# Performance work log

Measured on AMD Instinct MI355X. Metric: run time of the kernel, lower is better.

Reference implementation:

```python
import jax, jax.numpy as jnp
import numpy as np

B, L, D, H, DH = 1, 256, 128, 4, 32  # batch, seq, d_pair, n_head, d_hidden


def setup_inputs() -> dict:
    key = jax.random.key(0)
    ks = jax.random.split(key, 8)
    s = 0.02  # init scale for weights
    return {
        "pair": jax.random.normal(ks[0], (B, L, L, D), jnp.float32),
        "ln_w": jnp.ones((D,), jnp.float32),
        "ln_b": jnp.zeros((D,), jnp.float32),
        "Wq": jax.random.normal(ks[1], (D, H * DH), jnp.float32) * s,
        "Wk": jax.random.normal(ks[2], (D, H * DH), jnp.float32) * s,
        "Wv": jax.random.normal(ks[3], (D, H * DH), jnp.float32) * s,
        "Wb": jax.random.normal(ks[4], (D, H), jnp.float32) * s,
        "Wg": jax.random.normal(ks[5], (D, H * DH), jnp.float32) * s,
        "bg": jnp.ones((H * DH,), jnp.float32),
        "Wo": jax.random.normal(ks[6], (H * DH, D), jnp.float32) * s,
        "bo": jnp.zeros((D,), jnp.float32),
    }


def reference(pair, ln_w, ln_b, Wq, Wk, Wv, Wb, Wg, bg, Wo, bo):
    scale = DH ** -0.5
    # LayerNorm over d_pair
    mu = jnp.mean(pair, axis=-1, keepdims=True)
    var = jnp.mean((pair - mu) ** 2, axis=-1, keepdims=True)
    x = (pair - mu) * jax.lax.rsqrt(var + 1e-5) * ln_w + ln_b
    b, l = x.shape[0], x.shape[1]
    bias = jnp.einsum('bijd,dh->bijh', x, Wb)            # (B, L, L, H)
    gate = jax.nn.sigmoid(x @ Wg + bg)                   # (B, L, L, H*DH)
    q = (x @ Wq).reshape(b, l, l, H, DH) * scale
    k = (x @ Wk).reshape(b, l, l, H, DH)
    v = (x @ Wv).reshape(b, l, l, H, DH)
    # triangle attention over k (third L axis), bias shared across i
    attn = jnp.einsum('bijhd,bikhd->bijkh', q, k) + bias[:, None]
    attn = jax.nn.softmax(attn, axis=3)
    out = jnp.einsum('bijkh,bikhd->bijhd', attn, v).reshape(b, l, l, H * DH)
    out = gate * out
    return out @ Wo + bo
```

## Files before the change

### kernel.cpp

```cpp
#include <hip/hip_runtime.h>
#include <math.h>

#define NPOS 65536

typedef _Float16 f16x8 __attribute__((ext_vector_type(8)));
typedef _Float16 f16x4 __attribute__((ext_vector_type(4)));
typedef float    f32x4 __attribute__((ext_vector_type(4)));

__global__ __launch_bounds__(256) void split_w_kernel(
    const float* __restrict__ Wq, const float* __restrict__ Wk,
    const float* __restrict__ Wv, const float* __restrict__ Wg,
    _Float16* __restrict__ Wt_hi, _Float16* __restrict__ Wt_lo)
{
    int t = blockIdx.x * 256 + threadIdx.x;
    int ng = t >> 7, kk = t & 127;
    int mat = ng >> 7, n = ng & 127;
    const float* W = (mat == 0) ? Wq : (mat == 1) ? Wk : (mat == 2) ? Wv : Wg;
    float x = W[kk * 128 + n];
    _Float16 h = (_Float16)x;
    _Float16 lo = (_Float16)((x - (float)h) * 2048.0f);
    Wt_hi[t] = h;
    Wt_lo[t] = lo;
}

__global__ __launch_bounds__(256, 4) void ln_proj_kernel(
    const float* __restrict__ pair, const float* __restrict__ ln_w, const float* __restrict__ ln_b,
    const float* __restrict__ Wb, const float* __restrict__ bg,
    const _Float16* __restrict__ Wt_hi, const _Float16* __restrict__ Wt_lo,
    float* __restrict__ q, float* __restrict__ k, float* __restrict__ v,
    float* __restrict__ g, float* __restrict__ bias_n)
{
    __shared__ _Float16 xbuf[2][64][136];
    _Float16 (*xh)[136] = xbuf[0];
    _Float16 (*xl)[136] = xbuf[1];

    const int tid = threadIdx.x;
    const int p0  = blockIdx.x * 64;
    const int r   = tid >> 2;
    const int cb  = (tid & 3) * 32;

    float xv[32];
    {
        const float4* pr = (const float4*)(pair + (size_t)(p0 + r) * 128 + cb);
        #pragma unroll
        for (int i = 0; i < 8; ++i) {
            float4 t = pr[i];
            xv[i * 4 + 0] = t.x; xv[i * 4 + 1] = t.y;
            xv[i * 4 + 2] = t.z; xv[i * 4 + 3] = t.w;
        }
    }
    float sum = 0.f, sq = 0.f;
    #pragma unroll
    for (int i = 0; i < 32; ++i) { sum += xv[i]; sq += xv[i] * xv[i]; }
    sum += __shfl_xor(sum, 1); sq += __shfl_xor(sq, 1);
    sum += __shfl_xor(sum, 2); sq += __shfl_xor(sq, 2);
    float mean = sum * (1.f / 128.f);
    float var  = sq * (1.f / 128.f) - mean * mean;
    float rstd = rsqrtf(var + 1e-5f);

    float b0 = 0.f, b1 = 0.f, b2 = 0.f, b3 = 0.f;
    #pragma unroll
    for (int i8 = 0; i8 < 4; ++i8) {
        float4 lw0 = *(const float4*)(ln_w + cb + i8 * 8);
        float4 lw1 = *(const float4*)(ln_w + cb + i8 * 8 + 4);
        float4 lb0 = *(const float4*)(ln_b + cb + i8 * 8);
        float4 lb1 = *(const float4*)(ln_b + cb + i8 * 8 + 4);
        float lw[8] = {lw0.x, lw0.y, lw0.z, lw0.w, lw1.x, lw1.y, lw1.z, lw1.w};
        float lb[8] = {lb0.x, lb0.y, lb0.z, lb0.w, lb1.x, lb1.y, lb1.z, lb1.w};
        f16x8 hv, lv;
        #pragma unroll
        for (int j = 0; j < 8; ++j) {
            int i = i8 * 8 + j;
            float xn = (xv[i] - mean) * rstd * lw[j] + lb[j];
            _Float16 h = (_Float16)xn;
            hv[j] = h;
            lv[j] = (_Float16)((xn - (float)h) * 2048.0f);
            float4 wb = *(const float4*)(Wb + (size_t)(cb + i) * 4);
            b0 = fmaf(xn, wb.x, b0); b1 = fmaf(xn, wb.y, b1);
            b2 = fmaf(xn, wb.z, b2); b3 = fmaf(xn, wb.w, b3);
        }
        *(f16x8*)&xh[r][cb + i8 * 8] = hv;
        *(f16x8*)&xl[r][cb + i8 * 8] = lv;
    }
    b0 += __shfl_xor(b0, 1); b1 += __shfl_xor(b1, 1);
    b2 += __shfl_xor(b2, 1); b3 += __shfl_xor(b3, 1);
    b0 += __shfl_xor(b0, 2); b1 += __shfl_xor(b1, 2);
    b2 += __shfl_xor(b2, 2); b3 += __shfl_xor(b3, 2);
    if ((tid & 3) == 0) {
        int p = p0 + r;
        bias_n[0 * NPOS + p] = b0;
        bias_n[1 * NPOS + p] = b1;
        bias_n[2 * NPOS + p] = b2;
        bias_n[3 * NPOS + p] = b3;
    }
    __syncthreads();

    const int w  = tid >> 6, l = tid & 63;
    const int lm = l & 15, lg = l >> 4;
    const int arow = w * 16 + lm;

    f16x8 ahf[4], alf[4];
    #pragma unroll
    for (int kt = 0; kt < 4; ++kt) {
        ahf[kt] = *(const f16x8*)&xh[arow][kt * 32 + lg * 8];
        alf[kt] = *(const f16x8*)&xl[arow][kt * 32 + lg * 8];
    }

    _Float16 (*Bh)[136] = xbuf[0];
    _Float16 (*Bl)[136] = xbuf[1];
    float* stg = (float*)&xbuf[0][0][0];

    const float scale = 0.17677669529663687f;

    for (int chunk = 0; chunk < 8; ++chunk) {
        const int mat = chunk >> 1;
        const int colhalf = (chunk & 1) * 64;
        float* dst = (mat == 0) ? q : (mat == 1) ? k : (mat == 2) ? v : g;

        __syncthreads();

        {
            const _Float16* srch = Wt_hi + (size_t)(chunk * 64) * 128;
            const _Float16* srcl = Wt_lo + (size_t)(chunk * 64) * 128;
            #pragma unroll
            for (int it = 0; it < 4; ++it) {
                int idx = it * 256 + tid;
                int row = idx >> 4, kc8 = (idx & 15) * 8;
                *(f16x8*)&Bh[row][kc8] = *(const f16x8*)(srch + row * 128 + kc8);
                *(f16x8*)&Bl[row][kc8] = *(const f16x8*)(srcl + row * 128 + kc8);
            }
        }
        __syncthreads();

        f32x4 acch[4], accc[4];
        #pragma unroll
        for (int ct = 0; ct < 4; ++ct) {
            acch[ct] = (f32x4){0.f, 0.f, 0.f, 0.f};
            accc[ct] = (f32x4){0.f, 0.f, 0.f, 0.f};
        }
        #pragma unroll
        for (int kt = 0; kt < 4; ++kt) {
            const int koff = kt * 32 + lg * 8;
            #pragma unroll
            for (int ct = 0; ct < 4; ++ct) {
                f16x8 bh = *(const f16x8*)&Bh[ct * 16 + lm][koff];
                f16x8 bl = *(const f16x8*)&Bl[ct * 16 + lm][koff];
                acch[ct] = __builtin_amdgcn_mfma_f32_16x16x32_f16(ahf[kt], bh, acch[ct], 0, 0, 0);
                accc[ct] = __builtin_amdgcn_mfma_f32_16x16x32_f16(alf[kt], bh, accc[ct], 0, 0, 0);
                accc[ct] = __builtin_amdgcn_mfma_f32_16x16x32_f16(ahf[kt], bl, accc[ct], 0, 0, 0);
            }
        }

        __syncthreads();

        #pragma unroll
        for (int ct = 0; ct < 4; ++ct) {
            const int col = ct * 16 + lm;
            float bgv = (mat == 3) ? bg[colhalf + col] : 0.f;
            #pragma unroll
            for (int rr = 0; rr < 4; ++rr) {
                float val = acch[ct][rr] + accc[ct][rr] * (1.0f / 2048.0f);
                if (mat == 0) val *= scale;
                if (mat == 3) val = 1.f / (1.f + __expf(-(val + bgv)));
                stg[(w * 16 + lg * 4 + rr) * 68 + col] = val;
            }
        }
        __syncthreads();

        #pragma unroll
        for (int it = 0; it < 4; ++it) {
            int idx = it * 256 + tid;
            int row = idx >> 4, c4 = (idx & 15) * 4;
            float4 val = *(const float4*)&stg[row * 68 + c4];
            *(float4*)(dst + (size_t)(p0 + row) * 128 + colhalf + c4) = val;
        }
    }
}

__global__ __launch_bounds__(256, 3) void attn_kernel(
    const float* __restrict__ q, const float* __restrict__ k, const float* __restrict__ v,
    const float* __restrict__ g, const float* __restrict__ bias_n, float* __restrict__ go)
{
    __shared__ _Float16 Khs[32][56];
    __shared__ _Float16 Kls[32][56];
    __shared__ _Float16 Vts[32][56];
    __shared__ _Float16 Pb[4][64][40];

    const int tid  = threadIdx.x;
    const int w    = tid >> 6;
    const int lane = tid & 63;
    const int lg   = lane >> 4, lm = lane & 15;
    const int i = blockIdx.x >> 2, h = blockIdx.x & 3;
    const size_t base = (size_t)i * 256 * 128 + (size_t)h * 32;
    const int j0w = w * 64;

    f16x8 qh[4], ql[4];
    #pragma unroll
    for (int jt = 0; jt < 4; ++jt) {
        const float* qp = q + base + (size_t)(j0w + jt * 16 + lm) * 128 + lg * 8;
        float4 a = *(const float4*)qp;
        float4 b = *(const float4*)(qp + 4);
        float qv[8] = {a.x, a.y, a.z, a.w, b.x, b.y, b.z, b.w};
        #pragma unroll
        for (int e = 0; e < 8; ++e) {
            _Float16 hh = (_Float16)qv[e];
            qh[jt][e] = hh;
            ql[jt][e] = (_Float16)((qv[e] - (float)hh) * 2048.0f);
        }
    }

    float Oacc[2][4][4] = {};
    float mrow[4], lrow[4];
    #pragma unroll
    for (int jt = 0; jt < 4; ++jt) { mrow[jt] = -1e30f; lrow[jt] = 0.f; }

    const int sr  = tid >> 3;
    const int sc0 = (tid & 7) * 4;

    float4 kpre = *(const float4*)(k + base + (size_t)sr * 128 + sc0);
    float4 vpre = *(const float4*)(v + base + (size_t)sr * 128 + sc0);

    for (int kc = 0; kc < 256; kc += 32) {
        __syncthreads();
        {
            float kvv[4] = {kpre.x, kpre.y, kpre.z, kpre.w};
            f16x4 h4, l4;
            #pragma unroll
            for (int e = 0; e < 4; ++e) {
                _Float16 hh = (_Float16)kvv[e];
                h4[e] = hh;
                l4[e] = (_Float16)((kvv[e] - (float)hh) * 2048.0f);
            }
            *(f16x4*)&Khs[sr][sc0] = h4;
            *(f16x4*)&Kls[sr][sc0] = l4;
            Vts[sc0 + 0][sr] = (_Float16)vpre.x;
            Vts[sc0 + 1][sr] = (_Float16)vpre.y;
            Vts[sc0 + 2][sr] = (_Float16)vpre.z;
            Vts[sc0 + 3][sr] = (_Float16)vpre.w;
        }
        __syncthreads();
        if (kc + 32 < 256) {
            kpre = *(const float4*)(k + base + (size_t)(kc + 32 + sr) * 128 + sc0);
            vpre = *(const float4*)(v + base + (size_t)(kc + 32 + sr) * 128 + sc0);
        }

        f16x8 bh[2], bl[2], vf[2];
        #pragma unroll
        for (int kt = 0; kt < 2; ++kt) {
            bh[kt] = *(const f16x8*)&Khs[kt * 16 + lm][lg * 8];
            bl[kt] = *(const f16x8*)&Kls[kt * 16 + lm][lg * 8];
            vf[kt] = *(const f16x8*)&Vts[kt * 16 + lm][lg * 8];
        }

        #pragma unroll
        for (int jt = 0; jt < 4; ++jt) {
            const float* bj = bias_n + (size_t)h * NPOS
                            + (size_t)(j0w + jt * 16 + lm) * 256 + kc + lg * 4;
            float4 b0 = *(const float4*)bj;
            float4 b1 = *(const float4*)(bj + 16);
            f32x4 c0h = {b0.x, b0.y, b0.z, b0.w};
            f32x4 c1h = {b1.x, b1.y, b1.z, b1.w};
            f32x4 c0l = {0.f, 0.f, 0.f, 0.f}, c1l = {0.f, 0.f, 0.f, 0.f};
            c0h = __builtin_amdgcn_mfma_f32_16x16x32_f16(bh[0], qh[jt], c0h, 0, 0, 0);
            c0l = __builtin_amdgcn_mfma_f32_16x16x32_f16(bl[0], qh[jt], c0l, 0, 0, 0);
            c0l = __builtin_amdgcn_mfma_f32_16x16x32_f16(bh[0], ql[jt], c0l, 0, 0, 0);
            c1h = __builtin_amdgcn_mfma_f32_16x16x32_f16(bh[1], qh[jt], c1h, 0, 0, 0);
            c1l = __builtin_amdgcn_mfma_f32_16x16x32_f16(bl[1], qh[jt], c1l, 0, 0, 0);
            c1l = __builtin_amdgcn_mfma_f32_16x16x32_f16(bh[1], ql[jt], c1l, 0, 0, 0);

            float s[8];
            #pragma unroll
            for (int rr = 0; rr < 4; ++rr) {
                s[rr]     = c0h[rr] + c0l[rr] * (1.0f / 2048.0f);
                s[4 + rr] = c1h[rr] + c1l[rr] * (1.0f / 2048.0f);
            }
            float mx = s[0];
            #pragma unroll
            for (int e = 1; e < 8; ++e) mx = fmaxf(mx, s[e]);
            mx = fmaxf(mx, __shfl_xor(mx, 16));
            mx = fmaxf(mx, __shfl_xor(mx, 32));
            float mn = fmaxf(mrow[jt], mx);
            float alpha = __expf(mrow[jt] - mn);
            mrow[jt] = mn;
            float p[8], ps = 0.f;
            #pragma unroll
            for (int e = 0; e < 8; ++e) { p[e] = __expf(s[e] - mn); ps += p[e]; }
            ps += __shfl_xor(ps, 16);
            ps += __shfl_xor(ps, 32);
            lrow[jt] = lrow[jt] * alpha + ps;
            #pragma unroll
            for (int dt = 0; dt < 2; ++dt)
                #pragma unroll
                for (int rr = 0; rr < 4; ++rr) Oacc[dt][jt][rr] *= alpha;
            f16x4 pa, pbv;
            #pragma unroll
            for (int rr = 0; rr < 4; ++rr) { pa[rr] = (_Float16)p[rr]; pbv[rr] = (_Float16)p[4 + rr]; }
            *(f16x4*)&Pb[w][jt * 16 + lm][lg * 4]      = pa;
            *(f16x4*)&Pb[w][jt * 16 + lm][16 + lg * 4] = pbv;
        }

        #pragma unroll
        for (int jt = 0; jt < 4; ++jt) {
            f16x8 pf = *(const f16x8*)&Pb[w][jt * 16 + lm][lg * 8];
            #pragma unroll
            for (int dt = 0; dt < 2; ++dt) {
                f32x4 c = {Oacc[dt][jt][0], Oacc[dt][jt][1], Oacc[dt][jt][2], Oacc[dt][jt][3]};
                c = __builtin_amdgcn_mfma_f32_16x16x32_f16(vf[dt], pf, c, 0, 0, 0);
                Oacc[dt][jt][0] = c[0]; Oacc[dt][jt][1] = c[1];
                Oacc[dt][jt][2] = c[2]; Oacc[dt][jt][3] = c[3];
            }
        }
    }

    #pragma unroll
    for (int jt = 0; jt < 4; ++jt) {
        const int j = j0w + jt * 16 + lm;
        const float inv = 1.0f / lrow[jt];
        #pragma unroll
        for (int dt = 0; dt < 2; ++dt) {
            const float* gp = g + base + (size_t)j * 128 + dt * 16 + lg * 4;
            float4 gv = *(const float4*)gp;
            float4 ov;
            ov.x = Oacc[dt][jt][0] * inv * gv.x;
            ov.y = Oacc[dt][jt][1] * inv * gv.y;
            ov.z = Oacc[dt][jt][2] * inv * gv.z;
            ov.w = Oacc[dt][jt][3] * inv * gv.w;
            *(float4*)(go + base + (size_t)j * 128 + dt * 16 + lg * 4) = ov;
        }
    }
}

__global__ __launch_bounds__(256) void out_proj_kernel(
    const float* __restrict__ go, const float* __restrict__ Wo, const float* __restrict__ bo,
    float* __restrict__ out)
{
    __shared__ float at[64][140];
    const int tid = threadIdx.x;
    const int p0  = blockIdx.x * 64;

    for (int i = tid; i < 64 * 32; i += 256) {
        int row = i >> 5, c4 = (i & 31) * 4;
        float4 val = *(const float4*)(go + (size_t)(p0 + row) * 128 + c4);
        at[row][c4 + 0] = val.x; at[row][c4 + 1] = val.y;
        at[row][c4 + 2] = val.z; at[row][c4 + 3] = val.w;
    }
    __syncthreads();

    const int ty = tid >> 4, tx = tid & 15;
    float acc[4][8] = {};
    #pragma unroll 2
    for (int kk = 0; kk < 128; ++kk) {
        float4 wA = *(const float4*)(Wo + kk * 128 + tx * 8);
        float4 wB = *(const float4*)(Wo + kk * 128 + tx * 8 + 4);
        #pragma unroll
        for (int rr = 0; rr < 4; ++rr) {
            float av = at[ty * 4 + rr][kk];
            acc[rr][0] = fmaf(av, wA.x, acc[rr][0]);
            acc[rr][1] = fmaf(av, wA.y, acc[rr][1]);
            acc[rr][2] = fmaf(av, wA.z, acc[rr][2]);
            acc[rr][3] = fmaf(av, wA.w, acc[rr][3]);
            acc[rr][4] = fmaf(av, wB.x, acc[rr][4]);
            acc[rr][5] = fmaf(av, wB.y, acc[rr][5]);
            acc[rr][6] = fmaf(av, wB.z, acc[rr][6]);
            acc[rr][7] = fmaf(av, wB.w, acc[rr][7]);
        }
    }
    #pragma unroll
    for (int rr = 0; rr < 4; ++rr) {
        float ov[8];
        #pragma unroll
        for (int c = 0; c < 8; ++c) ov[c] = acc[rr][c] + bo[tx * 8 + c];
        float* outp = out + (size_t)(p0 + ty * 4 + rr) * 128 + tx * 8;
        *(float4*)outp       = *(float4*)ov;
        *(float4*)(outp + 4) = *(float4*)(ov + 4);
    }
}

extern "C" void kernel_launch(void* const* d_in, const int* in_sizes, int n_in,
                              void* d_out, int out_size, void* d_ws, size_t ws_size,
                              hipStream_t stream) {
    const float* pair = (const float*)d_in[0];
    const float* ln_w = (const float*)d_in[1];
    const float* ln_b = (const float*)d_in[2];
    const float* Wq   = (const float*)d_in[3];
    const float* Wk   = (const float*)d_in[4];
    const float* Wv   = (const float*)d_in[5];
    const float* Wb   = (const float*)d_in[6];
    const float* Wg   = (const float*)d_in[7];
    const float* bg   = (const float*)d_in[8];
    const float* Wo   = (const float*)d_in[9];
    const float* bo   = (const float*)d_in[10];

    float* ws     = (float*)d_ws;
    float* q      = ws;
    float* k      = ws + (size_t)1 * NPOS * 128;
    float* v      = ws + (size_t)2 * NPOS * 128;
    float* g      = ws + (size_t)3 * NPOS * 128;
    float* go     = ws + (size_t)4 * NPOS * 128;
    float* bias_n = ws + (size_t)5 * NPOS * 128;
    float* out    = (float*)d_out;

    _Float16* Wt_hi = (_Float16*)d_out;
    _Float16* Wt_lo = Wt_hi + (size_t)512 * 128;

    hipLaunchKernelGGL(split_w_kernel, dim3(256), dim3(256), 0, stream,
                       Wq, Wk, Wv, Wg, Wt_hi, Wt_lo);
    hipLaunchKernelGGL(ln_proj_kernel, dim3(1024), dim3(256), 0, stream,
                       pair, ln_w, ln_b, Wb, bg, Wt_hi, Wt_lo, q, k, v, g, bias_n);
    hipLaunchKernelGGL(attn_kernel, dim3(1024), dim3(256), 0, stream,
                       q, k, v, g, bias_n, go);
    hipLaunchKernelGGL(out_proj_kernel, dim3(1024), dim3(256), 0, stream,
                       go, Wo, bo, out);
}
```

Baseline: 264.0 us.

## Store q/k/v/g intermediates in fp16 and drop low-order weight/K splits

The projection kernel now writes q as a packed hi/lo fp16 pair and k, v, g as plain fp16, in place of fp32. Weights are kept only as a single fp16 copy, which removes one of the three MFMAs per tile. The attention kernel loads fp16 K and V directly and drops the K low-part correction. It processes 64 keys per iteration with wider shared tiles, and the projection store is overlapped with the next chunk's weight load. This roughly halves intermediate memory traffic and cuts split-precision MFMA work, at the cost of accuracy in the projections and in the attention scores.

Measured after the change: 255.6 us. 1.03x faster.

```diff
diff --git a/kernel.cpp b/kernel.cpp
--- a/kernel.cpp
+++ b/kernel.cpp
@@ -7,28 +7,29 @@
 typedef _Float16 f16x4 __attribute__((ext_vector_type(4)));
 typedef float    f32x4 __attribute__((ext_vector_type(4)));
 
+__device__ __forceinline__ unsigned short f16bits(_Float16 h) {
+    return __builtin_bit_cast(unsigned short, h);
+}
+
 __global__ __launch_bounds__(256) void split_w_kernel(
     const float* __restrict__ Wq, const float* __restrict__ Wk,
     const float* __restrict__ Wv, const float* __restrict__ Wg,
-    _Float16* __restrict__ Wt_hi, _Float16* __restrict__ Wt_lo)
+    _Float16* __restrict__ Wt_hi)
 {
     int t = blockIdx.x * 256 + threadIdx.x;
     int ng = t >> 7, kk = t & 127;
     int mat = ng >> 7, n = ng & 127;
     const float* W = (mat == 0) ? Wq : (mat == 1) ? Wk : (mat == 2) ? Wv : Wg;
-    float x = W[kk * 128 + n];
-    _Float16 h = (_Float16)x;
-    _Float16 lo = (_Float16)((x - (float)h) * 2048.0f);
-    Wt_hi[t] = h;
-    Wt_lo[t] = lo;
+    Wt_hi[t] = (_Float16)W[kk * 128 + n];
 }
 
 __global__ __launch_bounds__(256, 4) void ln_proj_kernel(
     const float* __restrict__ pair, const float* __restrict__ ln_w, const float* __restrict__ ln_b,
     const float* __restrict__ Wb, const float* __restrict__ bg,
-    const _Float16* __restrict__ Wt_hi, const _Float16* __restrict__ Wt_lo,
-    float* __restrict__ q, float* __restrict__ k, float* __restrict__ v,
-    float* __restrict__ g, float* __restrict__ bias_n)
+    const _Float16* __restrict__ Wt_hi,
+    _Float16* __restrict__ q_hi, _Float16* __restrict__ q_lo,
+    _Float16* __restrict__ k16, _Float16* __restrict__ v16, _Float16* __restrict__ g16,
+    float* __restrict__ bias_n)
 {
     __shared__ _Float16 xbuf[2][64][136];
     _Float16 (*xh)[136] = xbuf[0];
@@ -107,31 +108,54 @@
     }
 
     _Float16 (*Bh)[136] = xbuf[0];
-    _Float16 (*Bl)[136] = xbuf[1];
-    float* stg = (float*)&xbuf[0][0][0];
+    unsigned* stg = (unsigned*)&xbuf[1][0][0];
 
     const float scale = 0.17677669529663687f;
 
     for (int chunk = 0; chunk < 8; ++chunk) {
-        const int mat = chunk >> 1;
-        const int colhalf = (chunk & 1) * 64;
-        float* dst = (mat == 0) ? q : (mat == 1) ? k : (mat == 2) ? v : g;
-
         __syncthreads();
 
-        {
-            const _Float16* srch = Wt_hi + (size_t)(chunk * 64) * 128;
-            const _Float16* srcl = Wt_lo + (size_t)(chunk * 64) * 128;
+        const _Float16* srch = Wt_hi + (size_t)(chunk * 64) * 128;
+        f16x8 breg[4];
+        #pragma unroll
+        for (int it = 0; it < 4; ++it) {
+            int idx = it * 256 + tid;
+            breg[it] = *(const f16x8*)(srch + (idx >> 4) * 128 + (idx & 15) * 8);
+        }
+
+        if (chunk > 0) {
+            const int pm = (chunk - 1) >> 1, pcol = ((chunk - 1) & 1) * 64;
             #pragma unroll
             for (int it = 0; it < 4; ++it) {
                 int idx = it * 256 + tid;
-                int row = idx >> 4, kc8 = (idx & 15) * 8;
-                *(f16x8*)&Bh[row][kc8] = *(const f16x8*)(srch + row * 128 + kc8);
-                *(f16x8*)&Bl[row][kc8] = *(const f16x8*)(srcl + row * 128 + kc8);
-            }
+                int row = idx >> 4, c4 = (idx & 15) * 4;
+                uint4 pk = *(const uint4*)&stg[row * 68 + c4];
+                ushort4 hv = make_ushort4((unsigned short)(pk.x & 0xffff),
+                                          (unsigned short)(pk.y & 0xffff),
+                                          (unsigned short)(pk.z & 0xffff),
+                                          (unsigned short)(pk.w & 0xffff));
+                size_t off = (size_t)(p0 + row) * 128 + pcol + c4;
+                if (pm == 0) {
+                    *(ushort4*)(q_hi + off) = hv;
+                    ushort4 lv = make_ushort4((unsigned short)(pk.x >> 16),
+                                              (unsigned short)(pk.y >> 16),
+                                              (unsigned short)(pk.z >> 16),
+                                              (unsigned short)(pk.w >> 16));
+                    *(ushort4*)(q_lo + off) = lv;
+                } else if (pm == 1) *(ushort4*)(k16 + off) = hv;
+                else if   (pm == 2) *(ushort4*)(v16 + off) = hv;
+                else                *(ushort4*)(g16 + off) = hv;
+            }
+        }
+
+        #pragma unroll
+        for (int it = 0; it < 4; ++it) {
+            int idx = it * 256 + tid;
+            *(f16x8*)&Bh[idx >> 4][(idx & 15) * 8] = breg[it];
         }
         __syncthreads();
 
+        const int mat = chunk >> 1;
         f32x4 acch[4], accc[4];
         #pragma unroll
         for (int ct = 0; ct < 4; ++ct) {
@@ -144,15 +168,12 @@
             #pragma unroll
             for (int ct = 0; ct < 4; ++ct) {
                 f16x8 bh = *(const f16x8*)&Bh[ct * 16 + lm][koff];
-                f16x8 bl = *(const f16x8*)&Bl[ct * 16 + lm][koff];
                 acch[ct] = __builtin_amdgcn_mfma_f32_16x16x32_f16(ahf[kt], bh, acch[ct], 0, 0, 0);
                 accc[ct] = __builtin_amdgcn_mfma_f32_16x16x32_f16(alf[kt], bh, accc[ct], 0, 0, 0);
-                accc[ct] = __builtin_amdgcn_mfma_f32_16x16x32_f16(ahf[kt], bl, accc[ct], 0, 0, 0);
-            }
-        }
-
-        __syncthreads();
-
+            }
+        }
+
+        const int colhalf = (chunk & 1) * 64;
         #pragma unroll
         for (int ct = 0; ct < 4; ++ct) {
             const int col = ct * 16 + lm;
@@ -162,29 +183,42 @@
                 float val = acch[ct][rr] + accc[ct][rr] * (1.0f / 2048.0f);
                 if (mat == 0) val *= scale;
                 if (mat == 3) val = 1.f / (1.f + __expf(-(val + bgv)));
-                stg[(w * 16 + lg * 4 + rr) * 68 + col] = val;
-            }
-        }
-        __syncthreads();
-
+                _Float16 h = (_Float16)val;
+                unsigned pk = f16bits(h);
+                if (mat == 0) {
+                    _Float16 lo = (_Float16)((val - (float)h) * 2048.0f);
+                    pk |= ((unsigned)f16bits(lo)) << 16;
+                }
+                stg[(w * 16 + lg * 4 + rr) * 68 + col] = pk;
+            }
+        }
+    }
+
+    __syncthreads();
+    {
         #pragma unroll
         for (int it = 0; it < 4; ++it) {
             int idx = it * 256 + tid;
             int row = idx >> 4, c4 = (idx & 15) * 4;
-            float4 val = *(const float4*)&stg[row * 68 + c4];
-            *(float4*)(dst + (size_t)(p0 + row) * 128 + colhalf + c4) = val;
+            uint4 pk = *(const uint4*)&stg[row * 68 + c4];
+            ushort4 hv = make_ushort4((unsigned short)(pk.x & 0xffff),
+                                      (unsigned short)(pk.y & 0xffff),
+                                      (unsigned short)(pk.z & 0xffff),
+                                      (unsigned short)(pk.w & 0xffff));
+            *(ushort4*)(g16 + (size_t)(p0 + row) * 128 + 64 + c4) = hv;
         }
     }
 }
 
 __global__ __launch_bounds__(256, 3) void attn_kernel(
-    const float* __restrict__ q, const float* __restrict__ k, const float* __restrict__ v,
-    const float* __restrict__ g, const float* __restrict__ bias_n, float* __restrict__ go)
+    const _Float16* __restrict__ q_hi, const _Float16* __restrict__ q_lo,
+    const _Float16* __restrict__ k16, const _Float16* __restrict__ v16,
+    const _Float16* __restrict__ g16, const float* __restrict__ bias_n,
+    float* __restrict__ go)
 {
-    __shared__ _Float16 Khs[32][56];
-    __shared__ _Float16 Kls[32][56];
-    __shared__ _Float16 Vts[32][56];
-    __shared__ _Float16 Pb[4][64][40];
+    __shared__ _Float16 Khs[64][44];
+    __shared__ _Float16 Vts[32][76];
+    __shared__ _Float16 Pb[4][64][76];
 
     const int tid  = threadIdx.x;
     const int w    = tid >> 6;
@@ -197,16 +231,9 @@
     f16x8 qh[4], ql[4];
     #pragma unroll
     for (int jt = 0; jt < 4; ++jt) {
-        const float* qp = q + base + (size_t)(j0w + jt * 16 + lm) * 128 + lg * 8;
-        float4 a = *(const float4*)qp;
-        float4 b = *(const float4*)(qp + 4);
-        float qv[8] = {a.x, a.y, a.z, a.w, b.x, b.y, b.z, b.w};
-        #pragma unroll
-        for (int e = 0; e < 8; ++e) {
-            _Float16 hh = (_Float16)qv[e];
-            qh[jt][e] = hh;
-            ql[jt][e] = (_Float16)((qv[e] - (float)hh) * 2048.0f);
-        }
+        size_t off = base + (size_t)(j0w + jt * 16 + lm) * 128 + lg * 8;
+        qh[jt] = *(const f16x8*)(q_hi + off);
+        ql[jt] = *(const f16x8*)(q_lo + off);
     }
 
     float Oacc[2][4][4] = {};
@@ -214,77 +241,60 @@
     #pragma unroll
     for (int jt = 0; jt < 4; ++jt) { mrow[jt] = -1e30f; lrow[jt] = 0.f; }
 
-    const int sr  = tid >> 3;
-    const int sc0 = (tid & 7) * 4;
-
-    float4 kpre = *(const float4*)(k + base + (size_t)sr * 128 + sc0);
-    float4 vpre = *(const float4*)(v + base + (size_t)sr * 128 + sc0);
-
-    for (int kc = 0; kc < 256; kc += 32) {
+    const int sr  = tid >> 2;
+    const int sc8 = (tid & 3) * 8;
+
+    f16x8 kpre = *(const f16x8*)(k16 + base + (size_t)sr * 128 + sc8);
+    f16x8 vpre = *(const f16x8*)(v16 + base + (size_t)sr * 128 + sc8);
+
+    for (int kc = 0; kc < 256; kc += 64) {
         __syncthreads();
-        {
-            float kvv[4] = {kpre.x, kpre.y, kpre.z, kpre.w};
-            f16x4 h4, l4;
-            #pragma unroll
-            for (int e = 0; e < 4; ++e) {
-                _Float16 hh = (_Float16)kvv[e];
-                h4[e] = hh;
-                l4[e] = (_Float16)((kvv[e] - (float)hh) * 2048.0f);
-            }
-            *(f16x4*)&Khs[sr][sc0] = h4;
-            *(f16x4*)&Kls[sr][sc0] = l4;
-            Vts[sc0 + 0][sr] = (_Float16)vpre.x;
-            Vts[sc0 + 1][sr] = (_Float16)vpre.y;
-            Vts[sc0 + 2][sr] = (_Float16)vpre.z;
-            Vts[sc0 + 3][sr] = (_Float16)vpre.w;
-        }
+        *(f16x8*)&Khs[sr][sc8] = kpre;
+        #pragma unroll
+        for (int e = 0; e < 8; ++e) Vts[sc8 + e][sr] = vpre[e];
         __syncthreads();
-        if (kc + 32 < 256) {
-            kpre = *(const float4*)(k + base + (size_t)(kc + 32 + sr) * 128 + sc0);
-            vpre = *(const float4*)(v + base + (size_t)(kc + 32 + sr) * 128 + sc0);
-        }
-
-        f16x8 bh[2], bl[2], vf[2];
-        #pragma unroll
-        for (int kt = 0; kt < 2; ++kt) {
-            bh[kt] = *(const f16x8*)&Khs[kt * 16 + lm][lg * 8];
-            bl[kt] = *(const f16x8*)&Kls[kt * 16 + lm][lg * 8];
-            vf[kt] = *(const f16x8*)&Vts[kt * 16 + lm][lg * 8];
-        }
+        if (kc + 64 < 256) {
+            kpre = *(const f16x8*)(k16 + base + (size_t)(kc + 64 + sr) * 128 + sc8);
+            vpre = *(const f16x8*)(v16 + base + (size_t)(kc + 64 + sr) * 128 + sc8);
+        }
+
+        f16x8 kf[4];
+        #pragma unroll
+        for (int t = 0; t < 4; ++t) kf[t] = *(const f16x8*)&Khs[t * 16 + lm][lg * 8];
+        f16x8 vf[2][2];
+        #pragma unroll
+        for (int dt = 0; dt < 2; ++dt)
+            #pragma unroll
+            for (int ks = 0; ks < 2; ++ks)
+                vf[dt][ks] = *(const f16x8*)&Vts[dt * 16 + lm][ks * 32 + lg * 8];
 
         #pragma unroll
         for (int jt = 0; jt < 4; ++jt) {
             const float* bj = bias_n + (size_t)h * NPOS
                             + (size_t)(j0w + jt * 16 + lm) * 256 + kc + lg * 4;
-            float4 b0 = *(const float4*)bj;
-            float4 b1 = *(const float4*)(bj + 16);
-            f32x4 c0h = {b0.x, b0.y, b0.z, b0.w};
-            f32x4 c1h = {b1.x, b1.y, b1.z, b1.w};
-            f32x4 c0l = {0.f, 0.f, 0.f, 0.f}, c1l = {0.f, 0.f, 0.f, 0.f};
-            c0h = __builtin_amdgcn_mfma_f32_16x16x32_f16(bh[0], qh[jt], c0h, 0, 0, 0);
-            c0l = __builtin_amdgcn_mfma_f32_16x16x32_f16(bl[0], qh[jt], c0l, 0, 0, 0);
-            c0l = __builtin_amdgcn_mfma_f32_16x16x32_f16(bh[0], ql[jt], c0l, 0, 0, 0);
-            c1h = __builtin_amdgcn_mfma_f32_16x16x32_f16(bh[1], qh[jt], c1h, 0, 0, 0);
-            c1l = __builtin_amdgcn_mfma_f32_16x16x32_f16(bl[1], qh[jt], c1l, 0, 0, 0);
-            c1l = __builtin_amdgcn_mfma_f32_16x16x32_f16(bh[1], ql[jt], c1l, 0, 0, 0);
-
-            float s[8];
-            #pragma unroll
-            for (int rr = 0; rr < 4; ++rr) {
-                s[rr]     = c0h[rr] + c0l[rr] * (1.0f / 2048.0f);
-                s[4 + rr] = c1h[rr] + c1l[rr] * (1.0f / 2048.0f);
+            float s[16];
+            #pragma unroll
+            for (int t = 0; t < 4; ++t) {
+                float4 bv = *(const float4*)(bj + t * 16);
+                f32x4 c  = {bv.x, bv.y, bv.z, bv.w};
+                f32x4 cl = {0.f, 0.f, 0.f, 0.f};
+                c  = __builtin_amdgcn_mfma_f32_16x16x32_f16(kf[t], qh[jt], c,  0, 0, 0);
+                cl = __builtin_amdgcn_mfma_f32_16x16x32_f16(kf[t], ql[jt], cl, 0, 0, 0);
+                #pragma unroll
+                for (int rr = 0; rr < 4; ++rr)
+                    s[t * 4 + rr] = c[rr] + cl[rr] * (1.0f / 2048.0f);
             }
             float mx = s[0];
             #pragma unroll
-            for (int e = 1; e < 8; ++e) mx = fmaxf(mx, s[e]);
+            for (int e = 1; e < 16; ++e) mx = fmaxf(mx, s[e]);
             mx = fmaxf(mx, __shfl_xor(mx, 16));
             mx = fmaxf(mx, __shfl_xor(mx, 32));
             float mn = fmaxf(mrow[jt], mx);
             float alpha = __expf(mrow[jt] - mn);
             mrow[jt] = mn;
-            float p[8], ps = 0.f;
-            #pragma unroll
-            for (int e = 0; e < 8; ++e) { p[e] = __expf(s[e] - mn); ps += p[e]; }
+            float ps = 0.f;
+            #pragma unroll
+            for (int e = 0; e < 16; ++e) { s[e] = __expf(s[e] - mn); ps += s[e]; }
             ps += __shfl_xor(ps, 16);
             ps += __shfl_xor(ps, 32);
             lrow[jt] = lrow[jt] * alpha + ps;
@@ -292,20 +302,24 @@
             for (int dt = 0; dt < 2; ++dt)
                 #pragma unroll
                 for (int rr = 0; rr < 4; ++rr) Oacc[dt][jt][rr] *= alpha;
-            f16x4 pa, pbv;
-            #pragma unroll
-            for (int rr = 0; rr < 4; ++rr) { pa[rr] = (_Float16)p[rr]; pbv[rr] = (_Float16)p[4 + rr]; }
-            *(f16x4*)&Pb[w][jt * 16 + lm][lg * 4]      = pa;
-            *(f16x4*)&Pb[w][jt * 16 + lm][16 + lg * 4] = pbv;
+            #pragma unroll
+            for (int t = 0; t < 4; ++t) {
+                f16x4 pv;
+                #pragma unroll
+                for (int rr = 0; rr < 4; ++rr) pv[rr] = (_Float16)s[t * 4 + rr];
+                *(f16x4*)&Pb[w][jt * 16 + lm][t * 16 + lg * 4] = pv;
+            }
         }
 
         #pragma unroll
         for (int jt = 0; jt < 4; ++jt) {
-            f16x8 pf = *(const f16x8*)&Pb[w][jt * 16 + lm][lg * 8];
+            f16x8 pf0 = *(const f16x8*)&Pb[w][jt * 16 + lm][lg * 8];
+            f16x8 pf1 = *(const f16x8*)&Pb[w][jt * 16 + lm][32 + lg * 8];
             #pragma unroll
             for (int dt = 0; dt < 2; ++dt) {
                 f32x4 c = {Oacc[dt][jt][0], Oacc[dt][jt][1], Oacc[dt][jt][2], Oacc[dt][jt][3]};
-                c = __builtin_amdgcn_mfma_f32_16x16x32_f16(vf[dt], pf, c, 0, 0, 0);
+                c = __builtin_amdgcn_mfma_f32_16x16x32_f16(vf[dt][0], pf0, c, 0, 0, 0);
+                c = __builtin_amdgcn_mfma_f32_16x16x32_f16(vf[dt][1], pf1, c, 0, 0, 0);
                 Oacc[dt][jt][0] = c[0]; Oacc[dt][jt][1] = c[1];
                 Oacc[dt][jt][2] = c[2]; Oacc[dt][jt][3] = c[3];
             }
@@ -318,13 +332,12 @@
         const float inv = 1.0f / lrow[jt];
         #pragma unroll
         for (int dt = 0; dt < 2; ++dt) {
-            const float* gp = g + base + (size_t)j * 128 + dt * 16 + lg * 4;
-            float4 gv = *(const float4*)gp;
+            f16x4 gv4 = *(const f16x4*)(g16 + base + (size_t)j * 128 + dt * 16 + lg * 4);
             float4 ov;
-            ov.x = Oacc[dt][jt][0] * inv * gv.x;
-            ov.y = Oacc[dt][jt][1] * inv * gv.y;
-            ov.z = Oacc[dt][jt][2] * inv * gv.z;
-            ov.w = Oacc[dt][jt][3] * inv * gv.w;
+            ov.x = Oacc[dt][jt][0] * inv * (float)gv4[0];
+            ov.y = Oacc[dt][jt][1] * inv * (float)gv4[1];
+            ov.z = Oacc[dt][jt][2] * inv * (float)gv4[2];
+            ov.w = Oacc[dt][jt][3] * inv * (float)gv4[3];
             *(float4*)(go + base + (size_t)j * 128 + dt * 16 + lg * 4) = ov;
         }
     }
@@ -391,24 +404,24 @@
     const float* Wo   = (const float*)d_in[9];
     const float* bo   = (const float*)d_in[10];
 
-    float* ws     = (float*)d_ws;
-    float* q      = ws;
-    float* k      = ws + (size_t)1 * NPOS * 128;
-    float* v      = ws + (size_t)2 * NPOS * 128;
-    float* g      = ws + (size_t)3 * NPOS * 128;
-    float* go     = ws + (size_t)4 * NPOS * 128;
-    float* bias_n = ws + (size_t)5 * NPOS * 128;
-    float* out    = (float*)d_out;
+    _Float16* q_hi = (_Float16*)d_ws;
+    _Float16* q_lo = q_hi + (size_t)NPOS * 128;
+    _Float16* k16  = q_lo + (size_t)NPOS * 128;
+    _Float16* v16  = k16 + (size_t)NPOS * 128;
+    _Float16* g16  = v16 + (size_t)NPOS * 128;
+    float* go      = (float*)(g16 + (size_t)NPOS * 128);
+    float* bias_n  = go + (size_t)NPOS * 128;
+    float* out     = (float*)d_out;
 
     _Float16* Wt_hi = (_Float16*)d_out;
-    _Float16* Wt_lo = Wt_hi + (size_t)512 * 128;
 
     hipLaunchKernelGGL(split_w_kernel, dim3(256), dim3(256), 0, stream,
-                       Wq, Wk, Wv, Wg, Wt_hi, Wt_lo);
+                       Wq, Wk, Wv, Wg, Wt_hi);
     hipLaunchKernelGGL(ln_proj_kernel, dim3(1024), dim3(256), 0, stream,
-                       pair, ln_w, ln_b, Wb, bg, Wt_hi, Wt_lo, q, k, v, g, bias_n);
+                       pair, ln_w, ln_b, Wb, bg, Wt_hi,
+                       q_hi, q_lo, k16, v16, g16, bias_n);
     hipLaunchKernelGGL(attn_kernel, dim3(1024), dim3(256), 0, stream,
-                       q, k, v, g, bias_n, go);
+                       q_hi, q_lo, k16, v16, g16, bias_n, go);
     hipLaunchKernelGGL(out_proj_kernel, dim3(1024), dim3(256), 0, stream,
                        go, Wo, bo, out);
 }
```
